# Kernel optimization log

Measured on AMD Instinct MI355X. Metric: run time of the kernel, lower is better.

Reference implementation:

```python
import jax, jax.numpy as jnp
import numpy as np
from functools import partial

STEPLIM = 10
TOL = 1e-4


def _knn1(pc1, pc2):
    """1-NN of each point in pc1 (B,N1,3) against pc2 (B,N2,3).
    Same math as torch: L2 norm of broadcasted diff, topk(k=1, smallest),
    expressed via the |a|^2+|b|^2-2ab expansion to avoid the (B,N1,N2,3) diff."""
    sq1 = jnp.sum(pc1 * pc1, axis=-1)                       # (B,N1)
    sq2 = jnp.sum(pc2 * pc2, axis=-1)                       # (B,N2)
    cross = jnp.einsum('bnd,bmd->bnm', pc1, pc2)            # (B,N1,N2)
    d2 = jnp.maximum(sq1[..., :, None] + sq2[..., None, :] - 2.0 * cross, 0.0)
    idx = jnp.argmin(d2, axis=-1)                           # (B,N1)
    dmin = jnp.sqrt(jnp.take_along_axis(d2, idx[..., None], axis=-1)[..., 0])
    return dmin, idx


def _points_transform(pts1, pts2):
    """Kabsch/SVD rigid fit: R, t such that R @ pts1 + t ~= pts2 (EPnP._points_transform)."""
    c1 = jnp.mean(pts1, axis=-2, keepdims=True)             # (B,1,3)
    c2 = jnp.mean(pts2, axis=-2, keepdims=True)
    q1 = pts1 - c1
    q2 = pts2 - c2
    H = jnp.einsum('bni,bnj->bij', q1, q2)                  # (B,3,3) covariance
    U, S, Vh = jnp.linalg.svd(H)
    V = jnp.swapaxes(Vh, -1, -2)
    d = jnp.sign(jnp.linalg.det(jnp.einsum('bik,bjk->bij', V, U)))  # det(V U^T)
    sgn = jnp.stack([jnp.ones_like(d), jnp.ones_like(d), d], axis=-1)  # fix reflection
    R = jnp.einsum('bik,bk,bjk->bij', V, sgn, U)            # V diag(1,1,d) U^T
    t = c2 - jnp.einsum('bij,bnj->bni', R, c1)              # (B,1,3)
    return R, t


def _apply(R, t, pts):
    return jnp.einsum('bij,bnj->bni', R, pts) + t


def _icp(p1, p2):
    B = p1.shape[0]

    def step(carry, _):
        temppc, err, done = carry
        dmin, idx = _knn1(temppc, p2)
        errnew = jnp.mean(dmin, axis=-1)                    # (B,)
        # torch: first iteration err is None -> no break check; err0=inf makes cond False (nan < tol)
        cond = jnp.all(jnp.abs((errnew - err) / err) < TOL)
        new_done = done | cond
        matched = jax.vmap(lambda pc, i: pc[i])(p2, idx)    # (B,N1,3) gather of p2
        R, t = _points_transform(temppc, matched)
        temppc_new = _apply(R, t, temppc)
        temppc = jnp.where(new_done, temppc, temppc_new)
        err = jnp.where(new_done, err, errnew)
        return (temppc, err, new_done), None

    err0 = jnp.full((B,), jnp.inf, dtype=p1.dtype)
    done0 = jnp.array(False)
    (temppc, _, _), _ = jax.lax.scan(step, (p1, err0, done0), None, length=STEPLIM + 1)
    R, t = _points_transform(p1, temppc)
    return jnp.concatenate([R, jnp.swapaxes(t, -1, -2)], axis=-1)  # (B,3,4) = [R | t]


def setup_inputs() -> dict:
    key = jax.random.key(0)
    k1, k2 = jax.random.split(key)
    p1 = jax.random.normal(k1, (1, 8192, 3), dtype=jnp.float32)
    p2 = jax.random.normal(k2, (1, 8192, 3), dtype=jnp.float32)
    return {"p1": p1, "p2": p2}


def reference(p1, p2):
    return _icp(p1, p2)
```

## Files before the change

### kernel.cpp

```cpp
#include <hip/hip_runtime.h>
#include <float.h>
#include <math.h>

#define N_PTS 8192
#define NB    256
#define NT    1024
#define QPB   32
#define QPT   8
#define NRG   256
#define RC    32
#define STEPS 11
#define TOLV  1e-4

#define PADSLOT(i) ((i) + ((i) >> 6))
#define SC_SZ (N_PTS + N_PTS/64)
#define RBASE(r) (65*((r) >> 1) + 32*((r) & 1))

#define WS_P2F    0
#define WS_TEMPPC 131072
#define WS_BPA    229376
#define WS_BPB    262144
#define WS_ERRH   294912
#define WS_DONEH  295040

__device__ void kabsch3f(const float H[3][3], const float c1[3], const float c2[3],
                         float R[3][3], float t[3]) {
    float A[3][3];
    for (int i = 0; i < 3; ++i)
        for (int j = 0; j < 3; ++j) {
            float sacc = 0.0f;
            for (int k = 0; k < 3; ++k) sacc += H[k][i] * H[k][j];
            A[i][j] = sacc;
        }
    float V[3][3] = {{1,0,0},{0,1,0},{0,0,1}};
    for (int sweep = 0; sweep < 6; ++sweep) {
        const int PQ[3][2] = {{0,1},{0,2},{1,2}};
        for (int mm = 0; mm < 3; ++mm) {
            int p = PQ[mm][0], q = PQ[mm][1];
            float apq = A[p][q];
            if (fabsf(apq) < 1e-30f) continue;
            float app = A[p][p], aqq = A[q][q];
            float tau = (aqq - app) / (2.0f * apq);
            float tt = (tau >= 0.0f) ? 1.0f / (tau + sqrtf(1.0f + tau*tau))
                                     : 1.0f / (tau - sqrtf(1.0f + tau*tau));
            float c = 1.0f / sqrtf(1.0f + tt*tt), s = tt * c;
            A[p][p] = app - tt * apq;
            A[q][q] = aqq + tt * apq;
            A[p][q] = 0.0f; A[q][p] = 0.0f;
            int k = 3 - p - q;
            float akp = A[k][p], akq = A[k][q];
            A[k][p] = c*akp - s*akq; A[p][k] = A[k][p];
            A[k][q] = s*akp + c*akq; A[q][k] = A[k][q];
            for (int r = 0; r < 3; ++r) {
                float vp = V[r][p], vq = V[r][q];
                V[r][p] = c*vp - s*vq;
                V[r][q] = s*vp + c*vq;
            }
        }
    }
    float lam[3] = {A[0][0], A[1][1], A[2][2]};
    int ord[3] = {0,1,2};
    for (int i = 0; i < 2; ++i)
        for (int j = i+1; j < 3; ++j)
            if (lam[ord[j]] > lam[ord[i]]) { int tmp = ord[i]; ord[i] = ord[j]; ord[j] = tmp; }
    float v0[3] = {V[0][ord[0]], V[1][ord[0]], V[2][ord[0]]};
    float v1[3] = {V[0][ord[1]], V[1][ord[1]], V[2][ord[1]]};
    float v2[3] = {V[0][ord[2]], V[1][ord[2]], V[2][ord[2]]};

    float u0[3], u1[3], hv2[3];
    for (int i = 0; i < 3; ++i) u0[i] = H[i][0]*v0[0] + H[i][1]*v0[1] + H[i][2]*v0[2];
    float n0 = sqrtf(u0[0]*u0[0] + u0[1]*u0[1] + u0[2]*u0[2]);
    n0 = fmaxf(n0, 1e-30f);
    for (int i = 0; i < 3; ++i) u0[i] /= n0;

    for (int i = 0; i < 3; ++i) u1[i] = H[i][0]*v1[0] + H[i][1]*v1[1] + H[i][2]*v1[2];
    float d01 = u1[0]*u0[0] + u1[1]*u0[1] + u1[2]*u0[2];
    for (int i = 0; i < 3; ++i) u1[i] -= d01 * u0[i];
    float n1 = sqrtf(u1[0]*u1[0] + u1[1]*u1[1] + u1[2]*u1[2]);
    n1 = fmaxf(n1, 1e-30f);
    for (int i = 0; i < 3; ++i) u1[i] /= n1;

    float u2[3] = {u0[1]*u1[2] - u0[2]*u1[1],
                   u0[2]*u1[0] - u0[0]*u1[2],
                   u0[0]*u1[1] - u0[1]*u1[0]};
    for (int i = 0; i < 3; ++i) hv2[i] = H[i][0]*v2[0] + H[i][1]*v2[1] + H[i][2]*v2[2];
    if (hv2[0]*u2[0] + hv2[1]*u2[1] + hv2[2]*u2[2] < 0.0f) {
        v2[0] = -v2[0]; v2[1] = -v2[1]; v2[2] = -v2[2];
    }
    float cx = v1[1]*v2[2] - v1[2]*v2[1];
    float cy = v1[2]*v2[0] - v1[0]*v2[2];
    float cz = v1[0]*v2[1] - v1[1]*v2[0];
    float detV = v0[0]*cx + v0[1]*cy + v0[2]*cz;
    float dsg = (detV < 0.0f) ? -1.0f : 1.0f;

    for (int i = 0; i < 3; ++i)
        for (int j = 0; j < 3; ++j)
            R[i][j] = v0[i]*u0[j] + v1[i]*u1[j] + dsg * v2[i]*u2[j];
    for (int i = 0; i < 3; ++i)
        t[i] = c2[i] - (R[i][0]*c1[0] + R[i][1]*c1[1] + R[i][2]*c1[2]);
}

__device__ __forceinline__ void build_Hf(const double s[16], float c1[3], float c2[3],
                                         float H[3][3]) {
    const double Nn = (double)N_PTS;
    double c1d[3] = {s[1]/Nn, s[2]/Nn, s[3]/Nn};
    double c2d[3] = {s[4]/Nn, s[5]/Nn, s[6]/Nn};
    for (int i = 0; i < 3; ++i) { c1[i] = (float)c1d[i]; c2[i] = (float)c2d[i]; }
    for (int i = 0; i < 3; ++i)
        for (int j = 0; j < 3; ++j)
            H[i][j] = (float)(s[7 + 3*i + j] - Nn * c1d[i] * c2d[j]);
}

__device__ __forceinline__ float dist_val(float4 s, float mx, float my, float mz) {
    float v = fmaf(mx, s.x, s.w);
    v = fmaf(my, s.y, v);
    v = fmaf(mz, s.z, v);
    return v;
}

__global__ __launch_bounds__(NT, 4) void icp_scan(
    const float* __restrict__ p1, const float* __restrict__ p2,
    float4* __restrict__ p2f, float* __restrict__ temppc,
    const double* __restrict__ bp_prev, double* __restrict__ bp_cur,
    double* __restrict__ err_hist, int* __restrict__ done_hist, int it)
{
    __shared__ float4 sCand[SC_SZ];
    __shared__ float4 sQ[QPB];
    __shared__ float  sWmin[16][QPT];
    __shared__ int    sWin[QPB];
    __shared__ float  sRt[12];
    __shared__ int    sDone;
    const int tid = threadIdx.x, bid = blockIdx.x;

    if (it > 0 && done_hist[it-1]) {
        if (bid == 0 && tid == 0) { done_hist[it] = 1; err_hist[it] = err_hist[it-1]; }
        return;
    }

    if (tid < QPB) sWin[tid] = 0x7fffffff;

    if (it == 0) {
        #pragma unroll
        for (int k = 0; k < 8; ++k) {
            int i = tid + NT*k;
            float x = p2[3*i], y = p2[3*i+1], z = p2[3*i+2];
            sCand[PADSLOT(i)] = make_float4(x, y, z, x*x + y*y + z*z);
        }
        if (tid == 0) {
            sDone = 0;
            if (bid == 0) { err_hist[0] = __builtin_inf(); done_hist[0] = 0; }
        }
    } else {
        #pragma unroll
        for (int k = 0; k < 8; ++k) {
            int i = tid + NT*k;
            sCand[PADSLOT(i)] = p2f[i];
        }
        if (tid < 64) {
            double sv[16];
            #pragma unroll
            for (int k = 0; k < 16; ++k) sv[k] = 0.0;
            #pragma unroll
            for (int jj = 0; jj < 4; ++jj) {
                const double* row = bp_prev + (tid + 64*jj)*16;
                #pragma unroll
                for (int k = 0; k < 16; ++k) sv[k] += row[k];
            }
            #pragma unroll
            for (int off = 1; off < 64; off <<= 1) {
                #pragma unroll
                for (int k = 0; k < 16; ++k) sv[k] += __shfl_xor(sv[k], off, 64);
            }
            if (tid == 0) {
                double errnew = sv[0] / (double)N_PTS;
                double err = err_hist[it-1];
                double rel = fabs((errnew - err) / err);
                int nd = (rel < TOLV) ? 1 : 0;
                if (bid == 0) { done_hist[it] = nd; err_hist[it] = nd ? err : errnew; }
                sDone = nd;
                if (!nd) {
                    float c1[3], c2[3], H[3][3], Rm[3][3], tv[3];
                    build_Hf(sv, c1, c2, H);
                    kabsch3f(H, c1, c2, Rm, tv);
                    #pragma unroll
                    for (int i = 0; i < 3; ++i) {
                        sRt[3*i]   = Rm[i][0];
                        sRt[3*i+1] = Rm[i][1];
                        sRt[3*i+2] = Rm[i][2];
                        sRt[9+i]   = tv[i];
                    }
                }
            }
        }
    }
    __syncthreads();
    if (it > 0 && sDone) return;

    if (it == 0 && bid == 0) {
        #pragma unroll
        for (int k = 0; k < 8; ++k) {
            int i = tid + NT*k;
            p2f[i] = sCand[PADSLOT(i)];
        }
    }

    if (tid < QPB) {
        int q = bid*QPB + tid;
        float x, y, z;
        if (it == 0) {
            x = p1[3*q]; y = p1[3*q+1]; z = p1[3*q+2];
        } else {
            float ox = temppc[3*q], oy = temppc[3*q+1], oz = temppc[3*q+2];
            x = fmaf(sRt[0], ox, fmaf(sRt[1], oy, fmaf(sRt[2], oz, sRt[9])));
            y = fmaf(sRt[3], ox, fmaf(sRt[4], oy, fmaf(sRt[5], oz, sRt[10])));
            z = fmaf(sRt[6], ox, fmaf(sRt[7], oy, fmaf(sRt[8], oz, sRt[11])));
        }
        temppc[3*q] = x; temppc[3*q+1] = y; temppc[3*q+2] = z;
        sQ[tid] = make_float4(x, y, z, x*x + y*y + z*z);
    }
    __syncthreads();

    const int g = tid >> 8;
    const int r = tid & 255;
    float qx[QPT], qy[QPT], qz[QPT];
    #pragma unroll
    for (int k = 0; k < QPT; ++k) {
        float4 a = sQ[QPT*g + k];
        qx[k] = -2.f*a.x; qy[k] = -2.f*a.y; qz[k] = -2.f*a.z;
    }
    float tmin[QPT];
    #pragma unroll
    for (int k = 0; k < QPT; ++k) tmin[k] = FLT_MAX;
    const int sb = RBASE(r);
    float4 cur = sCand[sb];
    #pragma unroll 4
    for (int j = 0; j < RC - 1; ++j) {
        float4 nxt = sCand[sb + j + 1];
        #pragma unroll
        for (int k = 0; k < QPT; ++k)
            tmin[k] = fminf(tmin[k], dist_val(cur, qx[k], qy[k], qz[k]));
        cur = nxt;
    }
    #pragma unroll
    for (int k = 0; k < QPT; ++k)
        tmin[k] = fminf(tmin[k], dist_val(cur, qx[k], qy[k], qz[k]));

    float omin[QPT];
    #pragma unroll
    for (int k = 0; k < QPT; ++k) omin[k] = tmin[k];
    #pragma unroll
    for (int off = 1; off < 64; off <<= 1) {
        #pragma unroll
        for (int k = 0; k < QPT; ++k)
            tmin[k] = fminf(tmin[k], __shfl_xor(tmin[k], off, 64));
    }
    const int w = tid >> 6;
    if ((tid & 63) == 0) {
        #pragma unroll
        for (int k = 0; k < QPT; ++k) sWmin[w][k] = tmin[k];
    }
    __syncthreads();

    #pragma unroll
    for (int k = 0; k < QPT; ++k) {
        float gm = fminf(fminf(sWmin[4*g][k],   sWmin[4*g+1][k]),
                         fminf(sWmin[4*g+2][k], sWmin[4*g+3][k]));
        if (omin[k] == gm) atomicMin(&sWin[QPT*g + k], r);
    }
    __syncthreads();

    if (tid < 64) {
        double vals[16];
        if (tid < 32) {
            int q = tid, g2 = q >> 3, k2 = q & 7;
            float gm = fminf(fminf(sWmin[4*g2][k2],   sWmin[4*g2+1][k2]),
                             fminf(sWmin[4*g2+2][k2], sWmin[4*g2+3][k2]));
            int rw = sWin[q];
            float4 a4 = sQ[q];
            float mx = -2.f*a4.x, my = -2.f*a4.y, mz = -2.f*a4.z;
            int bix = -1;
            const int sbw = RBASE(rw);
            #pragma unroll 8
            for (int j = 0; j < RC; ++j) {
                float v = dist_val(sCand[sbw + j], mx, my, mz);
                if (v == gm && bix < 0) bix = RC*rw + j;
            }
            float d2 = fmaxf(gm + a4.w, 0.0f);
            float dmin = sqrtf(d2);
            float4 b4 = sCand[PADSLOT(bix)];
            vals[0] = (double)dmin;
            vals[1] = (double)a4.x; vals[2] = (double)a4.y; vals[3] = (double)a4.z;
            vals[4] = (double)b4.x; vals[5] = (double)b4.y; vals[6] = (double)b4.z;
            vals[7]  = (double)a4.x*b4.x; vals[8]  = (double)a4.x*b4.y; vals[9]  = (double)a4.x*b4.z;
            vals[10] = (double)a4.y*b4.x; vals[11] = (double)a4.y*b4.y; vals[12] = (double)a4.y*b4.z;
            vals[13] = (double)a4.z*b4.x; vals[14] = (double)a4.z*b4.y; vals[15] = (double)a4.z*b4.z;
        } else {
            #pragma unroll
            for (int k = 0; k < 16; ++k) vals[k] = 0.0;
        }
        #pragma unroll
        for (int off = 1; off < 32; off <<= 1) {
            #pragma unroll
            for (int k = 0; k < 16; ++k) vals[k] += __shfl_xor(vals[k], off, 64);
        }
        if (tid == 0) {
            double* d = bp_cur + bid*16;
            #pragma unroll
            for (int k = 0; k < 16; ++k) d[k] = vals[k];
        }
    }
}

#define FNT 512
__global__ __launch_bounds__(FNT) void icp_final(
    const float* __restrict__ p1, const float* __restrict__ temppc,
    const double* __restrict__ bp,
    const double* __restrict__ err_hist, const int* __restrict__ done_hist,
    float* __restrict__ out)
{
    __shared__ float  sRt[12];
    __shared__ int    sDone;
    __shared__ double sred[8][16];
    const int tid = threadIdx.x;

    if (tid < 64) {
        if (done_hist[STEPS-1]) {
            if (tid == 0) sDone = 1;
        } else {
            double sv[16];
            #pragma unroll
            for (int k = 0; k < 16; ++k) sv[k] = 0.0;
            #pragma unroll
            for (int jj = 0; jj < 4; ++jj) {
                const double* row = bp + (tid + 64*jj)*16;
                #pragma unroll
                for (int k = 0; k < 16; ++k) sv[k] += row[k];
            }
            #pragma unroll
            for (int off = 1; off < 64; off <<= 1) {
                #pragma unroll
                for (int k = 0; k < 16; ++k) sv[k] += __shfl_xor(sv[k], off, 64);
            }
            if (tid == 0) {
                double errnew = sv[0] / (double)N_PTS;
                double err = err_hist[STEPS-1];
                double rel = fabs((errnew - err) / err);
                int nd = (rel < TOLV) ? 1 : 0;
                sDone = nd;
                if (!nd) {
                    float c1[3], c2[3], H[3][3], Rm[3][3], tv[3];
                    build_Hf(sv, c1, c2, H);
                    kabsch3f(H, c1, c2, Rm, tv);
                    #pragma unroll
                    for (int i = 0; i < 3; ++i) {
                        sRt[3*i]   = Rm[i][0];
                        sRt[3*i+1] = Rm[i][1];
                        sRt[3*i+2] = Rm[i][2];
                        sRt[9+i]   = tv[i];
                    }
                }
            }
        }
    }
    __syncthreads();
    const int dn = sDone;

    double acc[16];
    #pragma unroll
    for (int k = 0; k < 16; ++k) acc[k] = 0.0;
    for (int i = tid; i < N_PTS; i += FNT) {
        float ax = p1[3*i], ay = p1[3*i+1], az = p1[3*i+2];
        float bx = temppc[3*i], by = temppc[3*i+1], bz = temppc[3*i+2];
        if (!dn) {
            float nx = fmaf(sRt[0], bx, fmaf(sRt[1], by, fmaf(sRt[2], bz, sRt[9])));
            float ny = fmaf(sRt[3], bx, fmaf(sRt[4], by, fmaf(sRt[5], bz, sRt[10])));
            float nz = fmaf(sRt[6], bx, fmaf(sRt[7], by, fmaf(sRt[8], bz, sRt[11])));
            bx = nx; by = ny; bz = nz;
        }
        acc[1] += (double)ax;  acc[2] += (double)ay;  acc[3] += (double)az;
        acc[4] += (double)bx;  acc[5] += (double)by;  acc[6] += (double)bz;
        acc[7]  += (double)ax*bx; acc[8]  += (double)ax*by; acc[9]  += (double)ax*bz;
        acc[10] += (double)ay*bx; acc[11] += (double)ay*by; acc[12] += (double)ay*bz;
        acc[13] += (double)az*bx; acc[14] += (double)az*by; acc[15] += (double)az*bz;
    }
    #pragma unroll
    for (int off = 1; off < 64; off <<= 1) {
        #pragma unroll
        for (int k = 0; k < 16; ++k) acc[k] += __shfl_xor(acc[k], off, 64);
    }
    const int w = tid >> 6;
    if ((tid & 63) == 0) {
        #pragma unroll
        for (int k = 0; k < 16; ++k) sred[w][k] = acc[k];
    }
    __syncthreads();
    if (tid == 0) {
        double sv[16];
        #pragma unroll
        for (int k = 0; k < 16; ++k) {
            double s = 0.0;
            #pragma unroll
            for (int ww = 0; ww < 8; ++ww) s += sred[ww][k];
            sv[k] = s;
        }
        float c1[3], c2[3], H[3][3], Rm[3][3], tv[3];
        build_Hf(sv, c1, c2, H);
        kabsch3f(H, c1, c2, Rm, tv);
        #pragma unroll
        for (int i = 0; i < 3; ++i) {
            out[4*i + 0] = Rm[i][0];
            out[4*i + 1] = Rm[i][1];
            out[4*i + 2] = Rm[i][2];
            out[4*i + 3] = tv[i];
        }
    }
}

extern "C" void kernel_launch(void* const* d_in, const int* in_sizes, int n_in,
                              void* d_out, int out_size, void* d_ws, size_t ws_size,
                              hipStream_t stream) {
    const float* p1 = (const float*)d_in[0];
    const float* p2 = (const float*)d_in[1];
    float* out = (float*)d_out;
    char* ws = (char*)d_ws;

    float4* p2f       = (float4*)(ws + WS_P2F);
    float*  temppc    = (float*) (ws + WS_TEMPPC);
    double* bpA       = (double*)(ws + WS_BPA);
    double* bpB       = (double*)(ws + WS_BPB);
    double* err_hist  = (double*)(ws + WS_ERRH);
    int*    done_hist = (int*)   (ws + WS_DONEH);

    for (int it = 0; it < STEPS; ++it) {
        double* cur  = (it & 1) ? bpB : bpA;
        double* prev = (it & 1) ? bpA : bpB;
        icp_scan<<<NB, NT, 0, stream>>>(p1, p2, p2f, temppc, prev, cur,
                                        err_hist, done_hist, it);
    }
    icp_final<<<1, FNT, 0, stream>>>(p1, temppc, bpA, err_hist, done_hist, out);
}
```

Measured before the change: 249.3 us.

## Pack candidate pairs into SoA float4 layout and use packed FMA for distances

Candidate points are stored as interleaved pairs (x0,x1,y0,y1)/(z0,z1,w0,w1) in two shared arrays so each thread evaluates two candidates per query with v_pk_fma_f32 instructions. This halves the FMA instruction count in the inner 1-NN scan. The winner recovery loop is rewritten to read from the paired layout and captures the matched coordinates directly. The early-exit on a latched done flag is moved later, so converged iterations now still load candidates before returning.

```diff
diff --git a/kernel.cpp b/kernel.cpp
--- a/kernel.cpp
+++ b/kernel.cpp
@@ -3,20 +3,24 @@
 #include <math.h>
 
 #define N_PTS 8192
+#define NPAIR 4096
 #define NB    256
 #define NT    1024
 #define QPB   32
 #define QPT   8
 #define NRG   256
+#define RPP   16
 #define RC    32
 #define STEPS 11
 #define TOLV  1e-4
 
-#define PADSLOT(i) ((i) + ((i) >> 6))
-#define SC_SZ (N_PTS + N_PTS/64)
-#define RBASE(r) (65*((r) >> 1) + 32*((r) & 1))
-
-#define WS_P2F    0
+#define PADP(p) ((p) + ((p) >> 4))
+#define SP_SZ (NPAIR + NPAIR/16)
+
+typedef float f32x2 __attribute__((ext_vector_type(2)));
+
+#define WS_PXY    0
+#define WS_PZW    65536
 #define WS_TEMPPC 131072
 #define WS_BPA    229376
 #define WS_BPB    262144
@@ -111,20 +115,21 @@
             H[i][j] = (float)(s[7 + 3*i + j] - Nn * c1d[i] * c2d[j]);
 }
 
-__device__ __forceinline__ float dist_val(float4 s, float mx, float my, float mz) {
-    float v = fmaf(mx, s.x, s.w);
-    v = fmaf(my, s.y, v);
-    v = fmaf(mz, s.z, v);
-    return v;
+__device__ __forceinline__ f32x2 pkfma(f32x2 a, f32x2 b, f32x2 c) {
+    f32x2 d;
+    asm("v_pk_fma_f32 %0, %1, %2, %3" : "=v"(d) : "v"(a), "v"(b), "v"(c));
+    return d;
 }
 
 __global__ __launch_bounds__(NT, 4) void icp_scan(
     const float* __restrict__ p1, const float* __restrict__ p2,
-    float4* __restrict__ p2f, float* __restrict__ temppc,
+    float4* __restrict__ pXY, float4* __restrict__ pZW,
+    float* __restrict__ temppc,
     const double* __restrict__ bp_prev, double* __restrict__ bp_cur,
     double* __restrict__ err_hist, int* __restrict__ done_hist, int it)
 {
-    __shared__ float4 sCand[SC_SZ];
+    __shared__ float4 sXY[SP_SZ];
+    __shared__ float4 sZW[SP_SZ];
     __shared__ float4 sQ[QPB];
     __shared__ float  sWmin[16][QPT];
     __shared__ int    sWin[QPB];
@@ -132,19 +137,18 @@
     __shared__ int    sDone;
     const int tid = threadIdx.x, bid = blockIdx.x;
 
-    if (it > 0 && done_hist[it-1]) {
-        if (bid == 0 && tid == 0) { done_hist[it] = 1; err_hist[it] = err_hist[it-1]; }
-        return;
-    }
-
     if (tid < QPB) sWin[tid] = 0x7fffffff;
 
     if (it == 0) {
         #pragma unroll
-        for (int k = 0; k < 8; ++k) {
-            int i = tid + NT*k;
-            float x = p2[3*i], y = p2[3*i+1], z = p2[3*i+2];
-            sCand[PADSLOT(i)] = make_float4(x, y, z, x*x + y*y + z*z);
+        for (int k = 0; k < 4; ++k) {
+            int p = tid + NT*k;
+            float x0 = p2[6*p],   y0 = p2[6*p+1], z0 = p2[6*p+2];
+            float x1 = p2[6*p+3], y1 = p2[6*p+4], z1 = p2[6*p+5];
+            sXY[PADP(p)] = make_float4(x0, x1, y0, y1);
+            sZW[PADP(p)] = make_float4(z0, z1,
+                                       x0*x0 + y0*y0 + z0*z0,
+                                       x1*x1 + y1*y1 + z1*z1);
         }
         if (tid == 0) {
             sDone = 0;
@@ -152,42 +156,51 @@
         }
     } else {
         #pragma unroll
-        for (int k = 0; k < 8; ++k) {
-            int i = tid + NT*k;
-            sCand[PADSLOT(i)] = p2f[i];
+        for (int k = 0; k < 4; ++k) {
+            int p = tid + NT*k;
+            sXY[PADP(p)] = pXY[p];
+            sZW[PADP(p)] = pZW[p];
         }
         if (tid < 64) {
+            const int latched = done_hist[it-1];
             double sv[16];
-            #pragma unroll
-            for (int k = 0; k < 16; ++k) sv[k] = 0.0;
-            #pragma unroll
-            for (int jj = 0; jj < 4; ++jj) {
-                const double* row = bp_prev + (tid + 64*jj)*16;
+            if (!latched) {
                 #pragma unroll
-                for (int k = 0; k < 16; ++k) sv[k] += row[k];
-            }
-            #pragma unroll
-            for (int off = 1; off < 64; off <<= 1) {
+                for (int k = 0; k < 16; ++k) sv[k] = 0.0;
                 #pragma unroll
-                for (int k = 0; k < 16; ++k) sv[k] += __shfl_xor(sv[k], off, 64);
+                for (int jj = 0; jj < 4; ++jj) {
+                    const double* row = bp_prev + (tid + 64*jj)*16;
+                    #pragma unroll
+                    for (int k = 0; k < 16; ++k) sv[k] += row[k];
+                }
+                #pragma unroll
+                for (int off = 1; off < 64; off <<= 1) {
+                    #pragma unroll
+                    for (int k = 0; k < 16; ++k) sv[k] += __shfl_xor(sv[k], off, 64);
+                }
             }
             if (tid == 0) {
-                double errnew = sv[0] / (double)N_PTS;
-                double err = err_hist[it-1];
-                double rel = fabs((errnew - err) / err);
-                int nd = (rel < TOLV) ? 1 : 0;
-                if (bid == 0) { done_hist[it] = nd; err_hist[it] = nd ? err : errnew; }
-                sDone = nd;
-                if (!nd) {
-                    float c1[3], c2[3], H[3][3], Rm[3][3], tv[3];
-                    build_Hf(sv, c1, c2, H);
-                    kabsch3f(H, c1, c2, Rm, tv);
-                    #pragma unroll
-                    for (int i = 0; i < 3; ++i) {
-                        sRt[3*i]   = Rm[i][0];
-                        sRt[3*i+1] = Rm[i][1];
-                        sRt[3*i+2] = Rm[i][2];
-                        sRt[9+i]   = tv[i];
+                if (latched) {
+                    if (bid == 0) { done_hist[it] = 1; err_hist[it] = err_hist[it-1]; }
+                    sDone = 1;
+                } else {
+                    double errnew = sv[0] / (double)N_PTS;
+                    double err = err_hist[it-1];
+                    double rel = fabs((errnew - err) / err);
+                    int nd = (rel < TOLV) ? 1 : 0;
+                    if (bid == 0) { done_hist[it] = nd; err_hist[it] = nd ? err : errnew; }
+                    sDone = nd;
+                    if (!nd) {
+                        float c1[3], c2[3], H[3][3], Rm[3][3], tv[3];
+                        build_Hf(sv, c1, c2, H);
+                        kabsch3f(H, c1, c2, Rm, tv);
+                        #pragma unroll
+                        for (int i = 0; i < 3; ++i) {
+                            sRt[3*i]   = Rm[i][0];
+                            sRt[3*i+1] = Rm[i][1];
+                            sRt[3*i+2] = Rm[i][2];
+                            sRt[9+i]   = tv[i];
+                        }
                     }
                 }
             }
@@ -198,9 +211,10 @@
 
     if (it == 0 && bid == 0) {
         #pragma unroll
-        for (int k = 0; k < 8; ++k) {
-            int i = tid + NT*k;
-            p2f[i] = sCand[PADSLOT(i)];
+        for (int k = 0; k < 4; ++k) {
+            int p = tid + NT*k;
+            pXY[p] = sXY[PADP(p)];
+            pZW[p] = sZW[PADP(p)];
         }
     }
 
@@ -222,32 +236,52 @@
 
     const int g = tid >> 8;
     const int r = tid & 255;
-    float qx[QPT], qy[QPT], qz[QPT];
+    f32x2 qx2[QPT], qy2[QPT], qz2[QPT];
     #pragma unroll
     for (int k = 0; k < QPT; ++k) {
         float4 a = sQ[QPT*g + k];
-        qx[k] = -2.f*a.x; qy[k] = -2.f*a.y; qz[k] = -2.f*a.z;
-    }
-    float tmin[QPT];
-    #pragma unroll
-    for (int k = 0; k < QPT; ++k) tmin[k] = FLT_MAX;
-    const int sb = RBASE(r);
-    float4 cur = sCand[sb];
-    #pragma unroll 4
-    for (int j = 0; j < RC - 1; ++j) {
-        float4 nxt = sCand[sb + j + 1];
-        #pragma unroll
-        for (int k = 0; k < QPT; ++k)
-            tmin[k] = fminf(tmin[k], dist_val(cur, qx[k], qy[k], qz[k]));
-        cur = nxt;
-    }
-    #pragma unroll
-    for (int k = 0; k < QPT; ++k)
-        tmin[k] = fminf(tmin[k], dist_val(cur, qx[k], qy[k], qz[k]));
-
-    float omin[QPT];
-    #pragma unroll
-    for (int k = 0; k < QPT; ++k) omin[k] = tmin[k];
+        float mx = -2.f*a.x, my = -2.f*a.y, mz = -2.f*a.z;
+        qx2[k].x = mx; qx2[k].y = mx;
+        qy2[k].x = my; qy2[k].y = my;
+        qz2[k].x = mz; qz2[k].y = mz;
+    }
+    f32x2 tmin2[QPT];
+    #pragma unroll
+    for (int k = 0; k < QPT; ++k) { tmin2[k].x = FLT_MAX; tmin2[k].y = FLT_MAX; }
+    const int base = 17*r;
+
+#define PROCP(XY, ZW)                                                   \
+    {                                                                   \
+        f32x2 sx2 = { (XY).x, (XY).y };                                 \
+        f32x2 sy2 = { (XY).z, (XY).w };                                 \
+        f32x2 sz2 = { (ZW).x, (ZW).y };                                 \
+        f32x2 sw2 = { (ZW).z, (ZW).w };                                 \
+        _Pragma("unroll")                                               \
+        for (int k = 0; k < QPT; ++k) {                                 \
+            f32x2 t = pkfma(qx2[k], sx2, sw2);                          \
+            t = pkfma(qy2[k], sy2, t);                                  \
+            t = pkfma(qz2[k], sz2, t);                                  \
+            tmin2[k].x = fminf(tmin2[k].x, t.x);                        \
+            tmin2[k].y = fminf(tmin2[k].y, t.y);                        \
+        }                                                               \
+    }
+
+    float4 xy = sXY[base], zw = sZW[base];
+    #pragma unroll 5
+    for (int j = 0; j < RPP - 1; ++j) {
+        float4 nxy = sXY[base + j + 1], nzw = sZW[base + j + 1];
+        PROCP(xy, zw);
+        xy = nxy; zw = nzw;
+    }
+    PROCP(xy, zw);
+#undef PROCP
+
+    float tmin[QPT], omin[QPT];
+    #pragma unroll
+    for (int k = 0; k < QPT; ++k) {
+        tmin[k] = fminf(tmin2[k].x, tmin2[k].y);
+        omin[k] = tmin[k];
+    }
     #pragma unroll
     for (int off = 1; off < 64; off <<= 1) {
         #pragma unroll
@@ -279,21 +313,30 @@
             float4 a4 = sQ[q];
             float mx = -2.f*a4.x, my = -2.f*a4.y, mz = -2.f*a4.z;
             int bix = -1;
-            const int sbw = RBASE(rw);
+            float bx = 0.f, by = 0.f, bz = 0.f;
+            const int pb = 17*rw;
             #pragma unroll 8
             for (int j = 0; j < RC; ++j) {
-                float v = dist_val(sCand[sbw + j], mx, my, mz);
-                if (v == gm && bix < 0) bix = RC*rw + j;
+                int pj = j >> 1, h = j & 1;
+                float4 cxy = sXY[pb + pj];
+                float4 czw = sZW[pb + pj];
+                float sx = h ? cxy.y : cxy.x;
+                float sy = h ? cxy.w : cxy.z;
+                float sz = h ? czw.y : czw.x;
+                float sw = h ? czw.w : czw.z;
+                float v = fmaf(mx, sx, sw);
+                v = fmaf(my, sy, v);
+                v = fmaf(mz, sz, v);
+                if (v == gm && bix < 0) { bix = RC*rw + j; bx = sx; by = sy; bz = sz; }
             }
             float d2 = fmaxf(gm + a4.w, 0.0f);
             float dmin = sqrtf(d2);
-            float4 b4 = sCand[PADSLOT(bix)];
             vals[0] = (double)dmin;
             vals[1] = (double)a4.x; vals[2] = (double)a4.y; vals[3] = (double)a4.z;
-            vals[4] = (double)b4.x; vals[5] = (double)b4.y; vals[6] = (double)b4.z;
-            vals[7]  = (double)a4.x*b4.x; vals[8]  = (double)a4.x*b4.y; vals[9]  = (double)a4.x*b4.z;
-            vals[10] = (double)a4.y*b4.x; vals[11] = (double)a4.y*b4.y; vals[12] = (double)a4.y*b4.z;
-            vals[13] = (double)a4.z*b4.x; vals[14] = (double)a4.z*b4.y; vals[15] = (double)a4.z*b4.z;
+            vals[4] = (double)bx;   vals[5] = (double)by;   vals[6] = (double)bz;
+            vals[7]  = (double)a4.x*bx; vals[8]  = (double)a4.x*by; vals[9]  = (double)a4.x*bz;
+            vals[10] = (double)a4.y*bx; vals[11] = (double)a4.y*by; vals[12] = (double)a4.y*bz;
+            vals[13] = (double)a4.z*bx; vals[14] = (double)a4.z*by; vals[15] = (double)a4.z*bz;
         } else {
             #pragma unroll
             for (int k = 0; k < 16; ++k) vals[k] = 0.0;
@@ -424,7 +467,8 @@
     float* out = (float*)d_out;
     char* ws = (char*)d_ws;
 
-    float4* p2f       = (float4*)(ws + WS_P2F);
+    float4* pXY       = (float4*)(ws + WS_PXY);
+    float4* pZW       = (float4*)(ws + WS_PZW);
     float*  temppc    = (float*) (ws + WS_TEMPPC);
     double* bpA       = (double*)(ws + WS_BPA);
     double* bpB       = (double*)(ws + WS_BPB);
@@ -434,7 +478,7 @@
     for (int it = 0; it < STEPS; ++it) {
         double* cur  = (it & 1) ? bpB : bpA;
         double* prev = (it & 1) ? bpA : bpB;
-        icp_scan<<<NB, NT, 0, stream>>>(p1, p2, p2f, temppc, prev, cur,
+        icp_scan<<<NB, NT, 0, stream>>>(p1, p2, pXY, pZW, temppc, prev, cur,
                                         err_hist, done_hist, it);
     }
     icp_final<<<1, FNT, 0, stream>>>(p1, temppc, bpA, err_hist, done_hist, out);
```

New measurement: 249.7 us, median of 2. No clear change (+0.2%).
